# Optimization experiments

Measured on AMD Instinct MI355X. Metric: run time of the kernel, lower is better.

Reference implementation:

```python
import jax, jax.numpy as jnp
import numpy as np


def _ln(x, g, b, eps=1e-5):
    m = x.mean(-1, keepdims=True)
    v = ((x - m) ** 2).mean(-1, keepdims=True)
    return (x - m) * jax.lax.rsqrt(v + eps) * g + b


def setup_inputs() -> dict:
    key = jax.random.key(0)
    ks = jax.random.split(key, 12)
    B, S, I, H, E, P, O, EM = 32, 512, 64, 512, 8, 96, 64, 512
    D = S * I
    r = lambda k, shape, s=0.02: jax.random.normal(k, shape, jnp.float32) * s
    z = lambda *shape: jnp.zeros(shape, jnp.float32)
    o = lambda *shape: jnp.ones(shape, jnp.float32)
    return dict(
        x=jax.random.normal(ks[0], (B, S, I), jnp.float32),
        gW1=r(ks[1], (D, EM)), gb1=z(EM), gln1_g=o(EM), gln1_b=z(EM),
        gW2=r(ks[2], (EM, EM)), gb2=z(EM), gln2_g=o(EM), gln2_b=z(EM),
        gW3=r(ks[3], (EM, 128)), gb3=z(128),
        protos=jax.random.normal(ks[4], (E, 128), jnp.float32) * 0.01,
        temp=jnp.ones((), jnp.float32),
        eW1=r(ks[5], (E, I, H)), eb1=z(E, H),
        eW2=r(ks[6], (E, H, H)), eb2=z(E, H),
        fW1=r(ks[7], (H, H)), fb1=z(H), fln_g=o(H), fln_b=z(H),
        fW2=r(ks[8], (H, H)), fb2=z(H),
        ln_g=o(H), ln_b=z(H),
        pW1=r(ks[9], (H, H // 2)), pb1=z(H // 2), pln_g=o(H // 2), pln_b=z(H // 2),
        pW2=r(ks[10], (H // 2, P * O)), pb2=z(P * O),
        on_g=o(O), on_b=z(O),
    )


def reference(x, gW1, gb1, gln1_g, gln1_b, gW2, gb2, gln2_g, gln2_b, gW3, gb3,
              protos, temp, eW1, eb1, eW2, eb2,
              fW1, fb1, fln_g, fln_b, fW2, fb2, ln_g, ln_b,
              pW1, pb1, pln_g, pln_b, pW2, pb2, on_g, on_b):
    B, S, I = x.shape
    O = on_g.shape[0]
    P = pW2.shape[1] // O
    # 1) flow latent mapping (identity fallback path of the original code)
    x_flat = x.reshape(B, S * I)
    z_latent = x_flat
    # 2) gating encoder -> 128-d embedding (dropout = identity in eval)
    h = jax.nn.relu(_ln(z_latent @ gW1 + gb1, gln1_g, gln1_b))
    h = jax.nn.relu(_ln(h @ gW2 + gb2, gln2_g, gln2_b))
    emb = h @ gW3 + gb3  # [B, 128]
    # 3) routing: euclidean cdist to prototypes, temperature-scaled softmax
    d2 = jnp.sum((emb[:, None, :] - protos[None, :, :]) ** 2, axis=-1)
    dist = jnp.sqrt(jnp.maximum(d2, 1e-12))  # [B, E]
    t = jnp.clip(temp, 0.1, 5.0)
    w = jax.nn.softmax(-dist / t, axis=-1)  # [B, E]
    # 4) experts: per-expert FFN on raw input, all experts batched
    he = jax.nn.relu(jnp.einsum('bsi,eih->besh', x, eW1) + eb1[None, :, None, :])
    eo = jnp.einsum('besh,eho->beso', he, eW2) + eb2[None, :, None, :]  # [B,E,S,H]
    # 5) routing-weighted combine + fusion + prediction head
    fused = jnp.einsum('besh,be->bsh', eo, w)
    f = jax.nn.relu(_ln(fused @ fW1 + fb1, fln_g, fln_b)) @ fW2 + fb2
    f = _ln(f, ln_g, ln_b)
    last = f[:, -1, :]  # [B, H]
    p = jax.nn.relu(_ln(last @ pW1 + pb1, pln_g, pln_b)) @ pW2 + pb2
    p = p.reshape(B, P, O)
    return _ln(p, on_g, on_b)
```

## Files before the change

kernel.cpp:

```cpp
#include <hip/hip_runtime.h>
#include <math.h>

#define DIMK 32768

__device__ __forceinline__ void fma4(float4& a, float s, const float4 w) {
  a.x += s * w.x; a.y += s * w.y; a.z += s * w.z; a.w += s * w.w;
}

__device__ __forceinline__ float block_sum(float v, float* red, int n) {
  int t = threadIdx.x;
  red[t] = v;
  __syncthreads();
  for (int s = n >> 1; s > 0; s >>= 1) {
    if (t < s) red[t] += red[t + s];
    __syncthreads();
  }
  float r = red[0];
  __syncthreads();
  return r;
}

__global__ __launch_bounds__(256) void gemm1(const float* __restrict__ x,
                                             const float* __restrict__ gW1,
                                             float* __restrict__ part) {
  const int mt = blockIdx.x, ks = blockIdx.y;
  const int m0 = mt * 128, k0 = ks * 256;
  const int t = threadIdx.x;
  __shared__ float As[32 * 260];
  __shared__ float Ws[64 * 128];

  for (int i = t; i < 2048; i += 256) {
    int b = i >> 6, q = i & 63;
    *(float4*)&As[b * 260 + q * 4] = *(const float4*)(x + (size_t)b * DIMK + k0 + q * 4);
  }
  const float* Wp = gW1 + (size_t)k0 * 512 + m0;
  float4 wreg[8];
#pragma unroll
  for (int j = 0; j < 8; ++j) {
    int i = t + j * 256, r = i >> 5, q = i & 31;
    wreg[j] = *(const float4*)(Wp + (size_t)r * 512 + q * 4);
  }

  const int mf = t & 31, bg = t >> 5;
  const int b0 = bg * 4;
  float4 acc[4];
#pragma unroll
  for (int j = 0; j < 4; ++j) acc[j] = make_float4(0.f, 0.f, 0.f, 0.f);
  const float* a0 = &As[b0 * 260];

  for (int s = 0; s < 4; ++s) {
    __syncthreads();
#pragma unroll
    for (int j = 0; j < 8; ++j) {
      int i = t + j * 256, r = i >> 5, q = i & 31;
      *(float4*)&Ws[r * 128 + q * 4] = wreg[j];
    }
    __syncthreads();
    if (s < 3) {
      const float* Wn = Wp + (size_t)(s + 1) * 64 * 512;
#pragma unroll
      for (int j = 0; j < 8; ++j) {
        int i = t + j * 256, r = i >> 5, q = i & 31;
        wreg[j] = *(const float4*)(Wn + (size_t)r * 512 + q * 4);
      }
    }
    const float* ab = a0 + s * 64;
#pragma unroll 8
    for (int k = 0; k < 64; ++k) {
      float4 wv = *(const float4*)&Ws[k * 128 + mf * 4];
      float av0 = ab[k], av1 = ab[260 + k], av2 = ab[520 + k], av3 = ab[780 + k];
      fma4(acc[0], av0, wv);
      fma4(acc[1], av1, wv);
      fma4(acc[2], av2, wv);
      fma4(acc[3], av3, wv);
    }
  }

  float* op = part + ((size_t)ks * 32 + b0) * 512 + m0 + mf * 4;
#pragma unroll
  for (int j = 0; j < 4; ++j) *(float4*)(op + (size_t)j * 512) = acc[j];
}

__global__ __launch_bounds__(512) void gred_ln(const float* __restrict__ part,
                                               const float* __restrict__ gb1,
                                               const float* __restrict__ g, const float* __restrict__ bt,
                                               float* __restrict__ h1) {
  const int b = blockIdx.x, t = threadIdx.x;
  __shared__ float red[512];
  float a = gb1[t];
  const float* pp0 = part + (size_t)b * 512 + t;
#pragma unroll 8
  for (int ks = 0; ks < 128; ++ks) a += pp0[(size_t)ks * 16384];
  float mean = block_sum(a, red, 512) * (1.f / 512.f);
  float d = a - mean;
  float var = block_sum(d * d, red, 512) * (1.f / 512.f);
  h1[b * 512 + t] = fmaxf(d * rsqrtf(var + 1e-5f) * g[t] + bt[t], 0.f);
}

template <int KC>
__global__ __launch_bounds__(256) void gemm_tile(const float* __restrict__ A,
                                                 const float* __restrict__ W,
                                                 float* __restrict__ outp,
                                                 int M, int aRow,
                                                 size_t aStrideE, size_t wStrideE) {
  const int mt = blockIdx.x, kq = blockIdx.y, e = blockIdx.z, NE = gridDim.z;
  const int m0 = mt * 64, k0 = kq * KC;
  const int t = threadIdx.x;
  __shared__ float Ws[KC * 64];
  __shared__ float As[32 * (KC + 4)];
  const float* Wp = W + (size_t)e * wStrideE + (size_t)k0 * M + m0;
  for (int i = t; i < KC * 16; i += 256) {
    int r = i >> 4, q = i & 15;
    *(float4*)&Ws[r * 64 + q * 4] = *(const float4*)(Wp + (size_t)r * M + q * 4);
  }
  const float* Ap = A + (size_t)e * aStrideE + k0;
  for (int i = t; i < 32 * (KC / 4); i += 256) {
    int b = i / (KC / 4), q = i % (KC / 4);
    *(float4*)&As[b * (KC + 4) + q * 4] = *(const float4*)(Ap + (size_t)b * aRow + q * 4);
  }
  __syncthreads();
  const int mf = t & 15, bg = t >> 4;
  const int b0 = bg * 2;
  float4 acc0 = make_float4(0.f, 0.f, 0.f, 0.f), acc1 = acc0;
  const float* a0 = &As[b0 * (KC + 4)];
  const float* a1 = &As[(b0 + 1) * (KC + 4)];
#pragma unroll 8
  for (int k = 0; k < KC; ++k) {
    float4 wv = *(const float4*)&Ws[k * 64 + mf * 4];
    fma4(acc0, a0[k], wv);
    fma4(acc1, a1[k], wv);
  }
  float* op = outp + ((size_t)(kq * NE + e) * 32 + b0) * M + m0 + mf * 4;
  *(float4*)op = acc0;
  *(float4*)(op + M) = acc1;
}

__global__ void red_ln(const float* __restrict__ zp, const float* __restrict__ bias,
                       const float* __restrict__ g, const float* __restrict__ bt,
                       float* __restrict__ outp, int M, int nq, int relu) {
  const int b = blockIdx.x, t = threadIdx.x;
  __shared__ float red[512];
  float a = bias[t];
#pragma unroll 4
  for (int kq = 0; kq < nq; ++kq) a += zp[((size_t)kq * 32 + b) * M + t];
  float fM = 1.f / (float)M;
  float mean = block_sum(a, red, M) * fM;
  float d = a - mean;
  float var = block_sum(d * d, red, M) * fM;
  float v = d * rsqrtf(var + 1e-5f) * g[t] + bt[t];
  outp[b * M + t] = relu ? fmaxf(v, 0.f) : v;
}

__global__ __launch_bounds__(128) void gate_k(const float* __restrict__ zp2,
                                              const float* __restrict__ gb3,
                                              const float* __restrict__ protos,
                                              const float* __restrict__ temp,
                                              float* __restrict__ wgt) {
  __shared__ float red[128];
  __shared__ float d2s[8];
  const int b = blockIdx.x, t = threadIdx.x;
  float a = gb3[t];
#pragma unroll 4
  for (int kq = 0; kq < 16; ++kq) a += zp2[((size_t)kq * 32 + b) * 128 + t];
  for (int e = 0; e < 8; ++e) {
    float dd = a - protos[e * 128 + t];
    float s = block_sum(dd * dd, red, 128);
    if (t == 0) d2s[e] = s;
  }
  __syncthreads();
  if (t == 0) {
    float tt = fminf(fmaxf(temp[0], 0.1f), 5.0f);
    float lg[8], mx = -1e30f;
#pragma unroll
    for (int e = 0; e < 8; ++e) {
      float dist = sqrtf(fmaxf(d2s[e], 1e-12f));
      lg[e] = -dist / tt;
      mx = fmaxf(mx, lg[e]);
    }
    float se = 0.f;
#pragma unroll
    for (int e = 0; e < 8; ++e) { lg[e] = expf(lg[e] - mx); se += lg[e]; }
#pragma unroll
    for (int e = 0; e < 8; ++e) wgt[b * 8 + e] = lg[e] / se;
  }
}

__global__ __launch_bounds__(256) void he_k(const float* __restrict__ x,
                                            const float* __restrict__ eW1,
                                            const float* __restrict__ eb1,
                                            float* __restrict__ he_all) {
  const int e = blockIdx.x, hs = blockIdx.y;
  const int t = threadIdx.x;
  __shared__ float xs[32 * 64];
  __shared__ float Ws[64 * 256];
  for (int i = t; i < 512; i += 256) {
    int b = i >> 4, q = i & 15;
    *(float4*)&xs[b * 64 + q * 4] = *(const float4*)(x + (size_t)b * DIMK + 32704 + q * 4);
  }
  const float* w1 = eW1 + (size_t)e * 64 * 512 + hs * 256;
  for (int i = t; i < 64 * 64; i += 256) {
    int k = i >> 6, q = i & 63;
    *(float4*)&Ws[k * 256 + q * 4] = *(const float4*)(w1 + (size_t)k * 512 + q * 4);
  }
  __syncthreads();
  float acc[32];
#pragma unroll
  for (int b = 0; b < 32; ++b) acc[b] = 0.f;
#pragma unroll 4
  for (int k = 0; k < 64; ++k) {
    float wk = Ws[k * 256 + t];
#pragma unroll
    for (int b = 0; b < 32; ++b) acc[b] += xs[b * 64 + k] * wk;
  }
  float bb = eb1[e * 512 + hs * 256 + t];
  for (int b = 0; b < 32; ++b)
    he_all[((size_t)e * 32 + b) * 512 + hs * 256 + t] = fmaxf(acc[b] + bb, 0.f);
}

__global__ __launch_bounds__(512) void ffuse(const float* __restrict__ epart,
                                             const float* __restrict__ eb2,
                                             const float* __restrict__ wgt,
                                             float* __restrict__ fused) {
  const int b = blockIdx.x, t = threadIdx.x;
  __shared__ float wl[8];
  if (t < 8) wl[t] = wgt[b * 8 + t];
  __syncthreads();
  float a = 0.f;
#pragma unroll
  for (int e = 0; e < 8; ++e) {
    float s = eb2[e * 512 + t];
#pragma unroll
    for (int kq = 0; kq < 8; ++kq)
      s += epart[(((size_t)kq * 8 + e) * 32 + b) * 512 + t];
    a += wl[e] * s;
  }
  fused[b * 512 + t] = a;
}

__global__ __launch_bounds__(256) void fin_red(const float* __restrict__ fpart,
                                               const float* __restrict__ pb2,
                                               const float* __restrict__ ong,
                                               const float* __restrict__ onb,
                                               float* __restrict__ outp) {
  const int t = threadIdx.x;
  const int lane = t & 63, w = t >> 6;
  const int r = blockIdx.x * 4 + w;
  const int b = r / 96, pi = r % 96;
  const int m = pi * 64 + lane;
  float a = pb2[m];
#pragma unroll
  for (int kq = 0; kq < 8; ++kq) a += fpart[((size_t)kq * 32 + b) * 6144 + m];
  float s = a;
  s += __shfl_xor(s, 1); s += __shfl_xor(s, 2); s += __shfl_xor(s, 4);
  s += __shfl_xor(s, 8); s += __shfl_xor(s, 16); s += __shfl_xor(s, 32);
  float mean = s * (1.f / 64.f);
  float d = a - mean;
  float q = d * d;
  q += __shfl_xor(q, 1); q += __shfl_xor(q, 2); q += __shfl_xor(q, 4);
  q += __shfl_xor(q, 8); q += __shfl_xor(q, 16); q += __shfl_xor(q, 32);
  float rr = rsqrtf(q * (1.f / 64.f) + 1e-5f);
  outp[((size_t)b * 96 + pi) * 64 + lane] = d * rr * ong[lane] + onb[lane];
}

extern "C" void kernel_launch(void* const* d_in, const int* in_sizes, int n_in,
                              void* d_out, int out_size, void* d_ws, size_t ws_size,
                              hipStream_t stream) {
  (void)in_sizes; (void)n_in; (void)out_size; (void)ws_size;
  const float* x      = (const float*)d_in[0];
  const float* gW1    = (const float*)d_in[1];
  const float* gb1    = (const float*)d_in[2];
  const float* gln1_g = (const float*)d_in[3];
  const float* gln1_b = (const float*)d_in[4];
  const float* gW2    = (const float*)d_in[5];
  const float* gb2    = (const float*)d_in[6];
  const float* gln2_g = (const float*)d_in[7];
  const float* gln2_b = (const float*)d_in[8];
  const float* gW3    = (const float*)d_in[9];
  const float* gb3    = (const float*)d_in[10];
  const float* protos = (const float*)d_in[11];
  const float* temp   = (const float*)d_in[12];
  const float* eW1    = (const float*)d_in[13];
  const float* eb1    = (const float*)d_in[14];
  const float* eW2    = (const float*)d_in[15];
  const float* eb2    = (const float*)d_in[16];
  const float* fW1    = (const float*)d_in[17];
  const float* fb1    = (const float*)d_in[18];
  const float* fln_g  = (const float*)d_in[19];
  const float* fln_b  = (const float*)d_in[20];
  const float* fW2    = (const float*)d_in[21];
  const float* fb2    = (const float*)d_in[22];
  const float* ln_g   = (const float*)d_in[23];
  const float* ln_b   = (const float*)d_in[24];
  const float* pW1    = (const float*)d_in[25];
  const float* pb1    = (const float*)d_in[26];
  const float* pln_g  = (const float*)d_in[27];
  const float* pln_b  = (const float*)d_in[28];
  const float* pW2    = (const float*)d_in[29];
  const float* pb2    = (const float*)d_in[30];
  const float* on_g   = (const float*)d_in[31];
  const float* on_b   = (const float*)d_in[32];
  float* out = (float*)d_out;

  float* ws     = (float*)d_ws;
  float* part   = ws;
  float* epart  = ws;
  float* he_all = ws + 1048576;
  float* fpart  = ws;
  float* h1     = ws + 2097152;
  float* h2     = h1 + 16384;
  float* zp     = h2 + 16384;
  float* zp2    = zp + 262144;
  float* wgt    = zp2 + 65536;
  float* fused  = wgt + 256;
  float* f1     = fused + 16384;
  float* lastv  = f1 + 16384;
  float* pp     = lastv + 16384;

  gemm1<<<dim3(4, 128), 256, 0, stream>>>(x, gW1, part);
  gred_ln<<<32, 512, 0, stream>>>(part, gb1, gln1_g, gln1_b, h1);
  gemm_tile<32><<<dim3(8, 16, 1), 256, 0, stream>>>(h1, gW2, zp, 512, 512, 0, 0);
  red_ln<<<32, 512, 0, stream>>>(zp, gb2, gln2_g, gln2_b, h2, 512, 16, 1);
  gemm_tile<32><<<dim3(2, 16, 1), 256, 0, stream>>>(h2, gW3, zp2, 128, 512, 0, 0);
  gate_k<<<32, 128, 0, stream>>>(zp2, gb3, protos, temp, wgt);

  he_k<<<dim3(8, 2), 256, 0, stream>>>(x, eW1, eb1, he_all);
  gemm_tile<64><<<dim3(8, 8, 8), 256, 0, stream>>>(he_all, eW2, epart, 512, 512,
                                                   (size_t)32 * 512, (size_t)512 * 512);
  ffuse<<<32, 512, 0, stream>>>(epart, eb2, wgt, fused);

  gemm_tile<32><<<dim3(8, 16, 1), 256, 0, stream>>>(fused, fW1, zp, 512, 512, 0, 0);
  red_ln<<<32, 512, 0, stream>>>(zp, fb1, fln_g, fln_b, f1, 512, 16, 1);
  gemm_tile<32><<<dim3(8, 16, 1), 256, 0, stream>>>(f1, fW2, zp, 512, 512, 0, 0);
  red_ln<<<32, 512, 0, stream>>>(zp, fb2, ln_g, ln_b, lastv, 512, 16, 0);
  gemm_tile<32><<<dim3(4, 16, 1), 256, 0, stream>>>(lastv, pW1, zp, 256, 512, 0, 0);
  red_ln<<<32, 256, 0, stream>>>(zp, pb1, pln_g, pln_b, pp, 256, 16, 1);

  gemm_tile<32><<<dim3(96, 8, 1), 256, 0, stream>>>(pp, pW2, fpart, 6144, 256, 0, 0);
  fin_red<<<768, 256, 0, stream>>>(fpart, pb2, on_g, on_b, out);
}
```

Before: 295.3 us.

## Fuse all stages into one persistent kernel with atomic grid barriers

Replaces the sixteen separate kernel launches with a single persistent kernel of 512 blocks. Stages are separated by a software grid barrier built on an atomic counter. The gate GEMM3, softmax and expert fuse are merged into one stage, and the expert work is reassigned to other blocks during the barrier phases. The aim is to remove launch overhead and inter-kernel gaps. The risks are that 512 resident blocks are required (a deadlock is avoided only by a timeout guard), and that many blocks sit idle at each barrier.

New measurement: 1.155 ms. 3.91x slower.

```diff
diff --git a/kernel.cpp b/kernel.cpp
--- a/kernel.cpp
+++ b/kernel.cpp
@@ -2,264 +2,388 @@
 #include <math.h>
 
 #define DIMK 32768
+#define NB 512
 
 __device__ __forceinline__ void fma4(float4& a, float s, const float4 w) {
   a.x += s * w.x; a.y += s * w.y; a.z += s * w.z; a.w += s * w.w;
 }
 
-__device__ __forceinline__ float block_sum(float v, float* red, int n) {
-  int t = threadIdx.x;
-  red[t] = v;
-  __syncthreads();
-  for (int s = n >> 1; s > 0; s >>= 1) {
-    if (t < s) red[t] += red[t + s];
-    __syncthreads();
-  }
-  float r = red[0];
-  __syncthreads();
-  return r;
-}
-
-__global__ __launch_bounds__(256) void gemm1(const float* __restrict__ x,
-                                             const float* __restrict__ gW1,
-                                             float* __restrict__ part) {
-  const int mt = blockIdx.x, ks = blockIdx.y;
-  const int m0 = mt * 128, k0 = ks * 256;
-  const int t = threadIdx.x;
-  __shared__ float As[32 * 260];
-  __shared__ float Ws[64 * 128];
-
+__device__ __forceinline__ void gsync(unsigned* bar, unsigned target) {
+  __syncthreads();
+  if (threadIdx.x == 0) {
+    __threadfence();
+    __hip_atomic_fetch_add(bar, 1u, __ATOMIC_RELEASE, __HIP_MEMORY_SCOPE_AGENT);
+    int guard = 0;
+    while (__hip_atomic_load(bar, __ATOMIC_ACQUIRE, __HIP_MEMORY_SCOPE_AGENT) < target) {
+      __builtin_amdgcn_s_sleep(2);
+      if (++guard > 4000000) break;
+    }
+    __threadfence();
+  }
+  __syncthreads();
+}
+
+__device__ __forceinline__ float bsum(float v, volatile float* r4) {
+  for (int o = 1; o < 64; o <<= 1) v += __shfl_xor(v, o);
+  const int w = threadIdx.x >> 6;
+  __syncthreads();
+  if ((threadIdx.x & 63) == 0) r4[w] = v;
+  __syncthreads();
+  return r4[0] + r4[1] + r4[2] + r4[3];
+}
+
+__device__ void redln512(const float* zp, const float* bias, const float* g,
+                         const float* bt, float* outp, int b, int nq, int relu,
+                         volatile float* r4) {
+  const int t = threadIdx.x;
+  float a0 = bias[t], a1 = bias[t + 256];
+  const float* p = zp + (size_t)b * 512;
+#pragma unroll 8
+  for (int kq = 0; kq < nq; ++kq) {
+    a0 += p[t]; a1 += p[t + 256];
+    p += 512 * 32;
+  }
+  float mean = bsum(a0 + a1, r4) * (1.f / 512.f);
+  float d0 = a0 - mean, d1 = a1 - mean;
+  float var = bsum(d0 * d0 + d1 * d1, r4) * (1.f / 512.f);
+  float rr = rsqrtf(var + 1e-5f);
+  float v0 = d0 * rr * g[t] + bt[t];
+  float v1 = d1 * rr * g[t + 256] + bt[t + 256];
+  outp[b * 512 + t] = relu ? fmaxf(v0, 0.f) : v0;
+  outp[b * 512 + t + 256] = relu ? fmaxf(v1, 0.f) : v1;
+}
+
+__device__ void redln256(const float* zp, const float* bias, const float* g,
+                         const float* bt, float* outp, int b, int nq, int relu,
+                         volatile float* r4) {
+  const int t = threadIdx.x;
+  float a = bias[t];
+  const float* p = zp + (size_t)b * 256 + t;
+#pragma unroll 8
+  for (int kq = 0; kq < nq; ++kq) { a += *p; p += 256 * 32; }
+  float mean = bsum(a, r4) * (1.f / 256.f);
+  float d = a - mean;
+  float var = bsum(d * d, r4) * (1.f / 256.f);
+  float v = d * rsqrtf(var + 1e-5f) * g[t] + bt[t];
+  outp[b * 256 + t] = relu ? fmaxf(v, 0.f) : v;
+}
+
+__device__ void sgemm32(const float* A, int aRow, const float* W, int M,
+                        float* outp, int mt, int kq, float* S) {
+  const int t = threadIdx.x;
+  const int m0 = mt * 32, k0 = kq * 32;
+  float* Ws = S;
+  float* As = S + 1024;
+  {
+    int r = t >> 3, q = t & 7;
+    *(float4*)&Ws[r * 32 + q * 4] = *(const float4*)(W + (size_t)(k0 + r) * M + m0 + q * 4);
+    *(float4*)&As[r * 36 + q * 4] = *(const float4*)(A + (size_t)r * aRow + k0 + q * 4);
+  }
+  __syncthreads();
+  const int b = t >> 3, mf = t & 7;
+  float4 acc = make_float4(0.f, 0.f, 0.f, 0.f);
+#pragma unroll
+  for (int k = 0; k < 32; ++k)
+    fma4(acc, As[b * 36 + k], *(const float4*)&Ws[k * 32 + mf * 4]);
+  *(float4*)(outp + ((size_t)kq * 32 + b) * M + m0 + mf * 4) = acc;
+  __syncthreads();
+}
+
+__device__ void egemm(const float* A, const float* W, float* outp,
+                      int mt, int kq, float* S) {
+  const int t = threadIdx.x;
+  const int m0 = mt * 64, k0 = kq * 128;
+  float* Ws = S;
+  float* As = S + 8192;
   for (int i = t; i < 2048; i += 256) {
-    int b = i >> 6, q = i & 63;
-    *(float4*)&As[b * 260 + q * 4] = *(const float4*)(x + (size_t)b * DIMK + k0 + q * 4);
-  }
-  const float* Wp = gW1 + (size_t)k0 * 512 + m0;
-  float4 wreg[8];
-#pragma unroll
-  for (int j = 0; j < 8; ++j) {
-    int i = t + j * 256, r = i >> 5, q = i & 31;
-    wreg[j] = *(const float4*)(Wp + (size_t)r * 512 + q * 4);
-  }
-
-  const int mf = t & 31, bg = t >> 5;
-  const int b0 = bg * 4;
-  float4 acc[4];
-#pragma unroll
-  for (int j = 0; j < 4; ++j) acc[j] = make_float4(0.f, 0.f, 0.f, 0.f);
-  const float* a0 = &As[b0 * 260];
-
-  for (int s = 0; s < 4; ++s) {
-    __syncthreads();
+    int r = i >> 4, q = i & 15;
+    *(float4*)&Ws[r * 64 + q * 4] = *(const float4*)(W + (size_t)(k0 + r) * 512 + m0 + q * 4);
+  }
+  for (int i = t; i < 1024; i += 256) {
+    int b = i >> 5, q = i & 31;
+    *(float4*)&As[b * 132 + q * 4] = *(const float4*)(A + (size_t)b * 512 + k0 + q * 4);
+  }
+  __syncthreads();
+  const int mf = t & 15, b0 = (t >> 4) * 2;
+  float4 a0 = make_float4(0.f, 0.f, 0.f, 0.f), a1 = a0;
+  const float* ar0 = As + b0 * 132;
+  const float* ar1 = ar0 + 132;
+#pragma unroll 4
+  for (int k = 0; k < 128; ++k) {
+    float4 wv = *(const float4*)&Ws[k * 64 + mf * 4];
+    fma4(a0, ar0[k], wv);
+    fma4(a1, ar1[k], wv);
+  }
+  float* op = outp + (size_t)b0 * 512 + m0 + mf * 4;
+  *(float4*)op = a0;
+  *(float4*)(op + 512) = a1;
+  __syncthreads();
+}
+
+__device__ void pgemm(const float* pp, const float* pW2, float* outp,
+                      int mt, int kq, float* S) {
+  const int t = threadIdx.x;
+  const int m0 = mt * 64, k0 = kq * 64;
+  float* Ws = S;
+  float* As = S + 4096;
+  for (int i = t; i < 1024; i += 256) {
+    int r = i >> 4, q = i & 15;
+    *(float4*)&Ws[r * 64 + q * 4] = *(const float4*)(pW2 + (size_t)(k0 + r) * 6144 + m0 + q * 4);
+  }
+  for (int i = t; i < 512; i += 256) {
+    int b = i >> 4, q = i & 15;
+    *(float4*)&As[b * 68 + q * 4] = *(const float4*)(pp + (size_t)b * 256 + k0 + q * 4);
+  }
+  __syncthreads();
+  const int mf = t & 15, b0 = (t >> 4) * 2;
+  float4 a0 = make_float4(0.f, 0.f, 0.f, 0.f), a1 = a0;
+  const float* ar0 = As + b0 * 68;
+  const float* ar1 = ar0 + 68;
+#pragma unroll 8
+  for (int k = 0; k < 64; ++k) {
+    float4 wv = *(const float4*)&Ws[k * 64 + mf * 4];
+    fma4(a0, ar0[k], wv);
+    fma4(a1, ar1[k], wv);
+  }
+  float* op = outp + (size_t)b0 * 6144 + m0 + mf * 4;
+  *(float4*)op = a0;
+  *(float4*)(op + 6144) = a1;
+  __syncthreads();
+}
+
+__global__ __launch_bounds__(256, 2) void mega(
+    const float* __restrict__ x, const float* __restrict__ gW1, const float* __restrict__ gb1,
+    const float* __restrict__ g1g, const float* __restrict__ g1b,
+    const float* __restrict__ gW2, const float* __restrict__ gb2,
+    const float* __restrict__ g2g, const float* __restrict__ g2b,
+    const float* __restrict__ gW3, const float* __restrict__ gb3,
+    const float* __restrict__ protos, const float* __restrict__ temp,
+    const float* __restrict__ eW1, const float* __restrict__ eb1,
+    const float* __restrict__ eW2, const float* __restrict__ eb2,
+    const float* __restrict__ fW1, const float* __restrict__ fb1,
+    const float* __restrict__ flg, const float* __restrict__ flb,
+    const float* __restrict__ fW2, const float* __restrict__ fb2,
+    const float* __restrict__ lng, const float* __restrict__ lnb,
+    const float* __restrict__ pW1, const float* __restrict__ pb1,
+    const float* __restrict__ plg, const float* __restrict__ plb,
+    const float* __restrict__ pW2, const float* __restrict__ pb2,
+    const float* __restrict__ ong, const float* __restrict__ onb,
+    float* __restrict__ ws, unsigned* __restrict__ bar,
+    float* __restrict__ outp) {
+  __shared__ __align__(16) float S[16512];
+  __shared__ float red4s[4];
+  __shared__ float aux[912];
+
+  float* part   = ws;
+  float* epart  = ws;
+  float* fpart  = ws;
+  float* he_all = ws + 2097152;
+  float* h1     = ws + 2228224;
+  float* h2     = h1 + 16384;
+  float* zp     = h2 + 16384;
+  float* fused  = zp + 262144;
+  float* f1     = fused + 16384;
+  float* lastv  = f1 + 16384;
+  float* pp     = lastv + 16384;
+
+  const int bid = blockIdx.x;
+  const int t = threadIdx.x;
+  unsigned phase = 0;
+
+  {
+    const int mt = bid & 3, ks = bid >> 2;
+    const int m0 = mt * 128, k0 = ks * 256;
+    float* As = S;
+    float* Ws = S + 8320;
+    for (int i = t; i < 2048; i += 256) {
+      int b = i >> 6, q = i & 63;
+      *(float4*)&As[b * 260 + q * 4] = *(const float4*)(x + (size_t)b * DIMK + k0 + q * 4);
+    }
+    const float* Wp = gW1 + (size_t)k0 * 512 + m0;
+    float4 wreg[8];
 #pragma unroll
     for (int j = 0; j < 8; ++j) {
       int i = t + j * 256, r = i >> 5, q = i & 31;
-      *(float4*)&Ws[r * 128 + q * 4] = wreg[j];
-    }
-    __syncthreads();
-    if (s < 3) {
-      const float* Wn = Wp + (size_t)(s + 1) * 64 * 512;
+      wreg[j] = *(const float4*)(Wp + (size_t)r * 512 + q * 4);
+    }
+    const int mf = t & 31, bg = t >> 5;
+    const int b0 = bg * 4;
+    float4 acc[4];
+#pragma unroll
+    for (int j = 0; j < 4; ++j) acc[j] = make_float4(0.f, 0.f, 0.f, 0.f);
+    const float* a0 = &As[b0 * 260];
+    for (int s = 0; s < 4; ++s) {
+      __syncthreads();
 #pragma unroll
       for (int j = 0; j < 8; ++j) {
         int i = t + j * 256, r = i >> 5, q = i & 31;
-        wreg[j] = *(const float4*)(Wn + (size_t)r * 512 + q * 4);
-      }
-    }
-    const float* ab = a0 + s * 64;
+        *(float4*)&Ws[r * 128 + q * 4] = wreg[j];
+      }
+      __syncthreads();
+      if (s < 3) {
+        const float* Wn = Wp + (size_t)(s + 1) * 64 * 512;
+#pragma unroll
+        for (int j = 0; j < 8; ++j) {
+          int i = t + j * 256, r = i >> 5, q = i & 31;
+          wreg[j] = *(const float4*)(Wn + (size_t)r * 512 + q * 4);
+        }
+      }
+      const float* ab = a0 + s * 64;
 #pragma unroll 8
-    for (int k = 0; k < 64; ++k) {
-      float4 wv = *(const float4*)&Ws[k * 128 + mf * 4];
-      float av0 = ab[k], av1 = ab[260 + k], av2 = ab[520 + k], av3 = ab[780 + k];
-      fma4(acc[0], av0, wv);
-      fma4(acc[1], av1, wv);
-      fma4(acc[2], av2, wv);
-      fma4(acc[3], av3, wv);
-    }
-  }
-
-  float* op = part + ((size_t)ks * 32 + b0) * 512 + m0 + mf * 4;
-#pragma unroll
-  for (int j = 0; j < 4; ++j) *(float4*)(op + (size_t)j * 512) = acc[j];
-}
-
-__global__ __launch_bounds__(512) void gred_ln(const float* __restrict__ part,
-                                               const float* __restrict__ gb1,
-                                               const float* __restrict__ g, const float* __restrict__ bt,
-                                               float* __restrict__ h1) {
-  const int b = blockIdx.x, t = threadIdx.x;
-  __shared__ float red[512];
-  float a = gb1[t];
-  const float* pp0 = part + (size_t)b * 512 + t;
+      for (int k = 0; k < 64; ++k) {
+        float4 wv = *(const float4*)&Ws[k * 128 + mf * 4];
+        fma4(acc[0], ab[k], wv);
+        fma4(acc[1], ab[260 + k], wv);
+        fma4(acc[2], ab[520 + k], wv);
+        fma4(acc[3], ab[780 + k], wv);
+      }
+    }
+    float* op = part + ((size_t)ks * 32 + b0) * 512 + m0 + mf * 4;
+#pragma unroll
+    for (int j = 0; j < 4; ++j) *(float4*)(op + (size_t)j * 512) = acc[j];
+  }
+  gsync(bar, ++phase * NB);
+
+  if (bid < 32) {
+    redln512(part, gb1, g1g, g1b, h1, bid, 128, 1, red4s);
+  } else if (bid < 48) {
+    const int e = (bid - 32) >> 1, hs = (bid - 32) & 1;
+    float* xs = S;
+    float* Ws = S + 2048;
+    for (int i = t; i < 512; i += 256) {
+      int b = i >> 4, q = i & 15;
+      *(float4*)&xs[b * 64 + q * 4] = *(const float4*)(x + (size_t)b * DIMK + 32704 + q * 4);
+    }
+    float acc[32];
+#pragma unroll
+    for (int b = 0; b < 32; ++b) acc[b] = 0.f;
+    for (int half = 0; half < 2; ++half) {
+      __syncthreads();
+      const float* w1 = eW1 + (size_t)e * 32768 + (size_t)(half * 32) * 512 + hs * 256;
+      for (int i = t; i < 2048; i += 256) {
+        int r = i >> 6, q = i & 63;
+        *(float4*)&Ws[r * 256 + q * 4] = *(const float4*)(w1 + (size_t)r * 512 + q * 4);
+      }
+      __syncthreads();
+#pragma unroll 4
+      for (int k = 0; k < 32; ++k) {
+        float wk = Ws[k * 256 + t];
+#pragma unroll
+        for (int b = 0; b < 32; ++b) acc[b] += xs[b * 64 + half * 32 + k] * wk;
+      }
+    }
+    float bb = eb1[e * 512 + hs * 256 + t];
+    for (int b = 0; b < 32; ++b)
+      he_all[((size_t)e * 32 + b) * 512 + hs * 256 + t] = fmaxf(acc[b] + bb, 0.f);
+  }
+  gsync(bar, ++phase * NB);
+
+  if (bid < 256) {
+    sgemm32(h1, 512, gW2, 512, zp, bid & 15, bid >> 4, S);
+  } else {
+    const int v = bid - 256;
+    const int kq = v >> 6, e = (v >> 3) & 7, mt = v & 7;
+    egemm(he_all + (size_t)e * 16384, eW2 + (size_t)e * 262144,
+          epart + ((size_t)(kq * 8 + e) * 32) * 512, mt, kq, S);
+  }
+  gsync(bar, ++phase * NB);
+
+  if (bid < 32) redln512(zp, gb2, g2g, g2b, h2, bid, 16, 1, red4s);
+  gsync(bar, ++phase * NB);
+
+  if (bid < 32) {
+    const int b = bid;
+    float* hb = aux;
+    float* emb = aux + 512;
+    float* embp = aux + 640;
+    float* wl = aux + 896;
+    float* d2s = aux + 904;
+    hb[t] = h2[b * 512 + t];
+    hb[t + 256] = h2[b * 512 + t + 256];
+    __syncthreads();
+    {
+      const int m = t & 127, kh = t >> 7;
+      float c = 0.f;
+      const float* w3 = gW3 + m;
 #pragma unroll 8
-  for (int ks = 0; ks < 128; ++ks) a += pp0[(size_t)ks * 16384];
-  float mean = block_sum(a, red, 512) * (1.f / 512.f);
-  float d = a - mean;
-  float var = block_sum(d * d, red, 512) * (1.f / 512.f);
-  h1[b * 512 + t] = fmaxf(d * rsqrtf(var + 1e-5f) * g[t] + bt[t], 0.f);
-}
-
-template <int KC>
-__global__ __launch_bounds__(256) void gemm_tile(const float* __restrict__ A,
-                                                 const float* __restrict__ W,
-                                                 float* __restrict__ outp,
-                                                 int M, int aRow,
-                                                 size_t aStrideE, size_t wStrideE) {
-  const int mt = blockIdx.x, kq = blockIdx.y, e = blockIdx.z, NE = gridDim.z;
-  const int m0 = mt * 64, k0 = kq * KC;
-  const int t = threadIdx.x;
-  __shared__ float Ws[KC * 64];
-  __shared__ float As[32 * (KC + 4)];
-  const float* Wp = W + (size_t)e * wStrideE + (size_t)k0 * M + m0;
-  for (int i = t; i < KC * 16; i += 256) {
-    int r = i >> 4, q = i & 15;
-    *(float4*)&Ws[r * 64 + q * 4] = *(const float4*)(Wp + (size_t)r * M + q * 4);
-  }
-  const float* Ap = A + (size_t)e * aStrideE + k0;
-  for (int i = t; i < 32 * (KC / 4); i += 256) {
-    int b = i / (KC / 4), q = i % (KC / 4);
-    *(float4*)&As[b * (KC + 4) + q * 4] = *(const float4*)(Ap + (size_t)b * aRow + q * 4);
-  }
-  __syncthreads();
-  const int mf = t & 15, bg = t >> 4;
-  const int b0 = bg * 2;
-  float4 acc0 = make_float4(0.f, 0.f, 0.f, 0.f), acc1 = acc0;
-  const float* a0 = &As[b0 * (KC + 4)];
-  const float* a1 = &As[(b0 + 1) * (KC + 4)];
-#pragma unroll 8
-  for (int k = 0; k < KC; ++k) {
-    float4 wv = *(const float4*)&Ws[k * 64 + mf * 4];
-    fma4(acc0, a0[k], wv);
-    fma4(acc1, a1[k], wv);
-  }
-  float* op = outp + ((size_t)(kq * NE + e) * 32 + b0) * M + m0 + mf * 4;
-  *(float4*)op = acc0;
-  *(float4*)(op + M) = acc1;
-}
-
-__global__ void red_ln(const float* __restrict__ zp, const float* __restrict__ bias,
-                       const float* __restrict__ g, const float* __restrict__ bt,
-                       float* __restrict__ outp, int M, int nq, int relu) {
-  const int b = blockIdx.x, t = threadIdx.x;
-  __shared__ float red[512];
-  float a = bias[t];
-#pragma unroll 4
-  for (int kq = 0; kq < nq; ++kq) a += zp[((size_t)kq * 32 + b) * M + t];
-  float fM = 1.f / (float)M;
-  float mean = block_sum(a, red, M) * fM;
-  float d = a - mean;
-  float var = block_sum(d * d, red, M) * fM;
-  float v = d * rsqrtf(var + 1e-5f) * g[t] + bt[t];
-  outp[b * M + t] = relu ? fmaxf(v, 0.f) : v;
-}
-
-__global__ __launch_bounds__(128) void gate_k(const float* __restrict__ zp2,
-                                              const float* __restrict__ gb3,
-                                              const float* __restrict__ protos,
-                                              const float* __restrict__ temp,
-                                              float* __restrict__ wgt) {
-  __shared__ float red[128];
-  __shared__ float d2s[8];
-  const int b = blockIdx.x, t = threadIdx.x;
-  float a = gb3[t];
-#pragma unroll 4
-  for (int kq = 0; kq < 16; ++kq) a += zp2[((size_t)kq * 32 + b) * 128 + t];
-  for (int e = 0; e < 8; ++e) {
-    float dd = a - protos[e * 128 + t];
-    float s = block_sum(dd * dd, red, 128);
-    if (t == 0) d2s[e] = s;
-  }
-  __syncthreads();
-  if (t == 0) {
-    float tt = fminf(fmaxf(temp[0], 0.1f), 5.0f);
-    float lg[8], mx = -1e30f;
-#pragma unroll
+      for (int k = kh * 256; k < kh * 256 + 256; ++k) c += hb[k] * w3[(size_t)k * 128];
+      embp[kh * 128 + m] = c;
+    }
+    __syncthreads();
+    if (t < 128) emb[t] = gb3[t] + embp[t] + embp[128 + t];
+    __syncthreads();
     for (int e = 0; e < 8; ++e) {
-      float dist = sqrtf(fmaxf(d2s[e], 1e-12f));
-      lg[e] = -dist / tt;
-      mx = fmaxf(mx, lg[e]);
-    }
-    float se = 0.f;
-#pragma unroll
-    for (int e = 0; e < 8; ++e) { lg[e] = expf(lg[e] - mx); se += lg[e]; }
-#pragma unroll
-    for (int e = 0; e < 8; ++e) wgt[b * 8 + e] = lg[e] / se;
-  }
-}
-
-__global__ __launch_bounds__(256) void he_k(const float* __restrict__ x,
-                                            const float* __restrict__ eW1,
-                                            const float* __restrict__ eb1,
-                                            float* __restrict__ he_all) {
-  const int e = blockIdx.x, hs = blockIdx.y;
-  const int t = threadIdx.x;
-  __shared__ float xs[32 * 64];
-  __shared__ float Ws[64 * 256];
-  for (int i = t; i < 512; i += 256) {
-    int b = i >> 4, q = i & 15;
-    *(float4*)&xs[b * 64 + q * 4] = *(const float4*)(x + (size_t)b * DIMK + 32704 + q * 4);
-  }
-  const float* w1 = eW1 + (size_t)e * 64 * 512 + hs * 256;
-  for (int i = t; i < 64 * 64; i += 256) {
-    int k = i >> 6, q = i & 63;
-    *(float4*)&Ws[k * 256 + q * 4] = *(const float4*)(w1 + (size_t)k * 512 + q * 4);
-  }
-  __syncthreads();
-  float acc[32];
-#pragma unroll
-  for (int b = 0; b < 32; ++b) acc[b] = 0.f;
-#pragma unroll 4
-  for (int k = 0; k < 64; ++k) {
-    float wk = Ws[k * 256 + t];
-#pragma unroll
-    for (int b = 0; b < 32; ++b) acc[b] += xs[b * 64 + k] * wk;
-  }
-  float bb = eb1[e * 512 + hs * 256 + t];
-  for (int b = 0; b < 32; ++b)
-    he_all[((size_t)e * 32 + b) * 512 + hs * 256 + t] = fmaxf(acc[b] + bb, 0.f);
-}
-
-__global__ __launch_bounds__(512) void ffuse(const float* __restrict__ epart,
-                                             const float* __restrict__ eb2,
-                                             const float* __restrict__ wgt,
-                                             float* __restrict__ fused) {
-  const int b = blockIdx.x, t = threadIdx.x;
-  __shared__ float wl[8];
-  if (t < 8) wl[t] = wgt[b * 8 + t];
-  __syncthreads();
-  float a = 0.f;
-#pragma unroll
-  for (int e = 0; e < 8; ++e) {
-    float s = eb2[e * 512 + t];
-#pragma unroll
-    for (int kq = 0; kq < 8; ++kq)
-      s += epart[(((size_t)kq * 8 + e) * 32 + b) * 512 + t];
-    a += wl[e] * s;
-  }
-  fused[b * 512 + t] = a;
-}
-
-__global__ __launch_bounds__(256) void fin_red(const float* __restrict__ fpart,
-                                               const float* __restrict__ pb2,
-                                               const float* __restrict__ ong,
-                                               const float* __restrict__ onb,
-                                               float* __restrict__ outp) {
-  const int t = threadIdx.x;
-  const int lane = t & 63, w = t >> 6;
-  const int r = blockIdx.x * 4 + w;
-  const int b = r / 96, pi = r % 96;
-  const int m = pi * 64 + lane;
-  float a = pb2[m];
-#pragma unroll
-  for (int kq = 0; kq < 8; ++kq) a += fpart[((size_t)kq * 32 + b) * 6144 + m];
-  float s = a;
-  s += __shfl_xor(s, 1); s += __shfl_xor(s, 2); s += __shfl_xor(s, 4);
-  s += __shfl_xor(s, 8); s += __shfl_xor(s, 16); s += __shfl_xor(s, 32);
-  float mean = s * (1.f / 64.f);
-  float d = a - mean;
-  float q = d * d;
-  q += __shfl_xor(q, 1); q += __shfl_xor(q, 2); q += __shfl_xor(q, 4);
-  q += __shfl_xor(q, 8); q += __shfl_xor(q, 16); q += __shfl_xor(q, 32);
-  float rr = rsqrtf(q * (1.f / 64.f) + 1e-5f);
-  outp[((size_t)b * 96 + pi) * 64 + lane] = d * rr * ong[lane] + onb[lane];
+      float dd = 0.f;
+      if (t < 128) { float z = emb[t] - protos[e * 128 + t]; dd = z * z; }
+      float s = bsum(dd, red4s);
+      if (t == 0) d2s[e] = s;
+    }
+    __syncthreads();
+    if (t == 0) {
+      float tt = fminf(fmaxf(temp[0], 0.1f), 5.0f);
+      float lg[8], mx = -1e30f;
+#pragma unroll
+      for (int e = 0; e < 8; ++e) {
+        float dist = sqrtf(fmaxf(d2s[e], 1e-12f));
+        lg[e] = -dist / tt;
+        mx = fmaxf(mx, lg[e]);
+      }
+      float se = 0.f;
+#pragma unroll
+      for (int e = 0; e < 8; ++e) { lg[e] = expf(lg[e] - mx); se += lg[e]; }
+#pragma unroll
+      for (int e = 0; e < 8; ++e) wl[e] = lg[e] / se;
+    }
+    __syncthreads();
+    float a0 = 0.f, a1 = 0.f;
+#pragma unroll
+    for (int e = 0; e < 8; ++e) {
+      float s0 = eb2[e * 512 + t], s1 = eb2[e * 512 + t + 256];
+#pragma unroll
+      for (int kq = 0; kq < 4; ++kq) {
+        const float* pe = epart + ((size_t)(kq * 8 + e) * 32 + b) * 512;
+        s0 += pe[t]; s1 += pe[t + 256];
+      }
+      a0 += wl[e] * s0; a1 += wl[e] * s1;
+    }
+    fused[b * 512 + t] = a0;
+    fused[b * 512 + t + 256] = a1;
+  }
+  gsync(bar, ++phase * NB);
+
+  if (bid < 256) sgemm32(fused, 512, fW1, 512, zp, bid & 15, bid >> 4, S);
+  gsync(bar, ++phase * NB);
+  if (bid < 32) redln512(zp, fb1, flg, flb, f1, bid, 16, 1, red4s);
+  gsync(bar, ++phase * NB);
+  if (bid < 256) sgemm32(f1, 512, fW2, 512, zp, bid & 15, bid >> 4, S);
+  gsync(bar, ++phase * NB);
+  if (bid < 32) redln512(zp, fb2, lng, lnb, lastv, bid, 16, 0, red4s);
+  gsync(bar, ++phase * NB);
+  if (bid < 128) sgemm32(lastv, 512, pW1, 256, zp, bid & 7, bid >> 3, S);
+  gsync(bar, ++phase * NB);
+  if (bid < 32) redln256(zp, pb1, plg, plb, pp, bid, 16, 1, red4s);
+  gsync(bar, ++phase * NB);
+  if (bid < 384) {
+    const int kq = bid / 96, mt = bid % 96;
+    pgemm(pp, pW2, fpart + (size_t)(kq * 32) * 6144, mt, kq, S);
+  }
+  gsync(bar, ++phase * NB);
+  for (int r0 = bid * 4 + (t >> 6); r0 < 3072; r0 += NB * 4) {
+    const int lane = t & 63;
+    const int b = r0 / 96, pi = r0 % 96;
+    const int m = pi * 64 + lane;
+    float a = pb2[m];
+#pragma unroll
+    for (int kq = 0; kq < 4; ++kq) a += fpart[((size_t)kq * 32 + b) * 6144 + m];
+    float s = a;
+    for (int o = 1; o < 64; o <<= 1) s += __shfl_xor(s, o);
+    float mean = s * (1.f / 64.f);
+    float d = a - mean;
+    float q = d * d;
+    for (int o = 1; o < 64; o <<= 1) q += __shfl_xor(q, o);
+    float rr = rsqrtf(q * (1.f / 64.f) + 1e-5f);
+    outp[(size_t)r0 * 64 + lane] = d * rr * ong[lane] + onb[lane];
+  }
 }
 
 extern "C" void kernel_launch(void* const* d_in, const int* in_sizes, int n_in,
@@ -301,40 +425,13 @@
   const float* on_b   = (const float*)d_in[32];
   float* out = (float*)d_out;
 
-  float* ws     = (float*)d_ws;
-  float* part   = ws;
-  float* epart  = ws;
-  float* he_all = ws + 1048576;
-  float* fpart  = ws;
-  float* h1     = ws + 2097152;
-  float* h2     = h1 + 16384;
-  float* zp     = h2 + 16384;
-  float* zp2    = zp + 262144;
-  float* wgt    = zp2 + 65536;
-  float* fused  = wgt + 256;
-  float* f1     = fused + 16384;
-  float* lastv  = f1 + 16384;
-  float* pp     = lastv + 16384;
-
-  gemm1<<<dim3(4, 128), 256, 0, stream>>>(x, gW1, part);
-  gred_ln<<<32, 512, 0, stream>>>(part, gb1, gln1_g, gln1_b, h1);
-  gemm_tile<32><<<dim3(8, 16, 1), 256, 0, stream>>>(h1, gW2, zp, 512, 512, 0, 0);
-  red_ln<<<32, 512, 0, stream>>>(zp, gb2, gln2_g, gln2_b, h2, 512, 16, 1);
-  gemm_tile<32><<<dim3(2, 16, 1), 256, 0, stream>>>(h2, gW3, zp2, 128, 512, 0, 0);
-  gate_k<<<32, 128, 0, stream>>>(zp2, gb3, protos, temp, wgt);
-
-  he_k<<<dim3(8, 2), 256, 0, stream>>>(x, eW1, eb1, he_all);
-  gemm_tile<64><<<dim3(8, 8, 8), 256, 0, stream>>>(he_all, eW2, epart, 512, 512,
-                                                   (size_t)32 * 512, (size_t)512 * 512);
-  ffuse<<<32, 512, 0, stream>>>(epart, eb2, wgt, fused);
-
-  gemm_tile<32><<<dim3(8, 16, 1), 256, 0, stream>>>(fused, fW1, zp, 512, 512, 0, 0);
-  red_ln<<<32, 512, 0, stream>>>(zp, fb1, fln_g, fln_b, f1, 512, 16, 1);
-  gemm_tile<32><<<dim3(8, 16, 1), 256, 0, stream>>>(f1, fW2, zp, 512, 512, 0, 0);
-  red_ln<<<32, 512, 0, stream>>>(zp, fb2, ln_g, ln_b, lastv, 512, 16, 0);
-  gemm_tile<32><<<dim3(4, 16, 1), 256, 0, stream>>>(lastv, pW1, zp, 256, 512, 0, 0);
-  red_ln<<<32, 256, 0, stream>>>(zp, pb1, pln_g, pln_b, pp, 256, 16, 1);
-
-  gemm_tile<32><<<dim3(96, 8, 1), 256, 0, stream>>>(pp, pW2, fpart, 6144, 256, 0, 0);
-  fin_red<<<768, 256, 0, stream>>>(fpart, pb2, on_g, on_b, out);
-}
+  float* ws = (float*)d_ws;
+  unsigned* bar = (unsigned*)(ws + 2580608);
+
+  hipMemsetAsync((void*)bar, 0, 64, stream);
+  mega<<<NB, 256, 0, stream>>>(x, gW1, gb1, gln1_g, gln1_b, gW2, gb2, gln2_g, gln2_b,
+                               gW3, gb3, protos, temp, eW1, eb1, eW2, eb2,
+                               fW1, fb1, fln_g, fln_b, fW2, fb2, ln_g, ln_b,
+                               pW1, pb1, pln_g, pln_b, pW2, pb2, on_g, on_b,
+                               ws, bar, out);
+}
```
